# Performance work log

Measured on AMD Instinct MI355X. Metric: run time of the kernel, lower is better.

Reference implementation:

```python
import jax, jax.numpy as jnp
import numpy as np

N_NODES = 50000
HIDDEN = 128
N_REL = 9
N_LAYERS = 3
N_EDGES = 600000


def setup_inputs() -> dict:
    key = jax.random.key(0)
    k1, k2, k3, k4, k5 = jax.random.split(key, 5)
    edge_index = jax.random.randint(k1, (2, N_EDGES), 0, N_NODES, dtype=jnp.int64 if jax.config.jax_enable_x64 else jnp.int32)
    edge_type = jax.random.randint(k2, (N_EDGES,), 0, N_REL, dtype=edge_index.dtype)
    embeddings = jax.random.uniform(k3, (N_NODES, HIDDEN), dtype=jnp.float32)
    weights = jax.random.uniform(k4, (N_LAYERS, N_REL, HIDDEN, HIDDEN), dtype=jnp.float32)
    biases = jax.random.uniform(k5, (N_LAYERS, N_REL, HIDDEN), dtype=jnp.float32)
    return {"edge_index": edge_index, "edge_type": edge_type,
            "embeddings": embeddings, "weights": weights, "biases": biases}


def reference(edge_index, edge_type, embeddings, weights, biases):
    # RGCN: per relation r, messages = emb[src] @ W[l,r] + b[l,r], scatter-summed
    # into dest. Equivalent vectorized form: precompute X = emb @ W for all
    # relations ([R,N,E]), then a single gather + segment_sum over edges.
    L = weights.shape[0]
    N = embeddings.shape[0]
    dest = edge_index[0]
    src = edge_index[1]
    out = embeddings
    for l in range(L):
        X = jnp.einsum('ne,ref->rnf', out, weights[l])        # [R, N, E]
        msg = X[edge_type, src] + biases[l][edge_type]        # [num_edges, E]
        hidden = jax.ops.segment_sum(msg, dest, num_segments=N)  # [N, E]
        if l + 1 < L:
            hidden = jax.nn.relu(hidden)
        out = hidden
    return out
```

## Files before the change

### kernel.cpp

```cpp
#include <hip/hip_runtime.h>

#define NNODES 50000
#define HID 128
#define NREL 9
#define NLAYERS 3
#define NEDGES 600000

#define NBINS (NREL * NNODES)
#define SCAN_CHUNK 1024
#define NBLK ((NBINS + SCAN_CHUNK - 1) / SCAN_CHUNK)

#define KTOT (NREL * HID)
#define GM2 32
#define FPITCH 136

typedef __attribute__((ext_vector_type(8))) short short8;
typedef __attribute__((ext_vector_type(4))) float f32x4;

__device__ __forceinline__ short f2bf(float f) {
    union { float f; unsigned u; } c; c.f = f;
    unsigned r = c.u + 0x7fff + ((c.u >> 16) & 1);
    return (short)(r >> 16);
}
__device__ __forceinline__ float bf2f(short v) {
    return __uint_as_float(((unsigned)(unsigned short)v) << 16);
}


__global__ void hist2_kernel(const int* __restrict__ dst, const int* __restrict__ etype,
                             int* __restrict__ bins) {
    int e = blockIdx.x * blockDim.x + threadIdx.x;
    if (e < NEDGES) {
        int bin = etype[e] * NNODES + dst[e];
        atomicAdd(&bins[bin], 1);
    }
}

__global__ __launch_bounds__(256) void scan_pass1(const int* __restrict__ bins,
                                                  int* __restrict__ blocksum) {
    __shared__ int red[256];
    int b = blockIdx.x, t = threadIdx.x;
    int i0 = b * SCAN_CHUNK + t * 4;
    int s = 0;
#pragma unroll
    for (int k = 0; k < 4; k++)
        if (i0 + k < NBINS) s += bins[i0 + k];
    red[t] = s;
    __syncthreads();
    for (int off = 128; off > 0; off >>= 1) {
        if (t < off) red[t] += red[t + off];
        __syncthreads();
    }
    if (t == 0) blocksum[b] = red[0];
}

__global__ __launch_bounds__(512) void scan_pass2(const int* __restrict__ blocksum,
                                                  int* __restrict__ blockoff,
                                                  int* __restrict__ rowptr) {
    __shared__ int s[512];
    int t = threadIdx.x;
    int v = (t < NBLK) ? blocksum[t] : 0;
    s[t] = v;
    __syncthreads();
    for (int off = 1; off < 512; off <<= 1) {
        int x = (t >= off) ? s[t - off] : 0;
        __syncthreads();
        s[t] += x;
        __syncthreads();
    }
    if (t < NBLK) blockoff[t] = s[t] - v;
    if (t == 0) rowptr[NBINS] = NEDGES;
}

__global__ __launch_bounds__(256) void scan_pass3(const int* __restrict__ bins,
                                                  const int* __restrict__ blockoff,
                                                  int* __restrict__ rowptr,
                                                  int* __restrict__ cursor) {
    __shared__ int sc[256];
    int b = blockIdx.x, t = threadIdx.x;
    int i0 = b * SCAN_CHUNK + t * 4;
    int v[4], p[4];
    int s = 0;
#pragma unroll
    for (int k = 0; k < 4; k++) {
        v[k] = (i0 + k < NBINS) ? bins[i0 + k] : 0;
        p[k] = s;
        s += v[k];
    }
    sc[t] = s;
    __syncthreads();
    for (int off = 1; off < 256; off <<= 1) {
        int x = (t >= off) ? sc[t - off] : 0;
        __syncthreads();
        sc[t] += x;
        __syncthreads();
    }
    int base = blockoff[b] + (sc[t] - s);
#pragma unroll
    for (int k = 0; k < 4; k++) {
        if (i0 + k < NBINS) {
            rowptr[i0 + k] = base + p[k];
            cursor[i0 + k] = base + p[k];
        }
    }
}

__global__ void place_kernel(const int* __restrict__ dst, const int* __restrict__ src,
                             const int* __restrict__ etype,
                             int* __restrict__ cursor, int* __restrict__ bsrc) {
    int e = blockIdx.x * blockDim.x + threadIdx.x;
    if (e < NEDGES) {
        int bin = etype[e] * NNODES + dst[e];
        int pos = atomicAdd(&cursor[bin], 1);
        bsrc[pos] = src[e];
    }
}


__global__ __launch_bounds__(256) void convert_w(const float* __restrict__ W,
                                                 short* __restrict__ Wt2) {
    int lr = blockIdx.x;
    int l = lr / NREL, r = lr - l * NREL;
    const float* w = W + (size_t)lr * HID * HID;
    short* o = Wt2 + (size_t)l * HID * KTOT;
    int tid = threadIdx.x;
#pragma unroll 4
    for (int i = 0; i < 64; i++) {
        int elem = i * 256 + tid;
        int kk = elem >> 7, n = elem & 127;
        o[(size_t)n * KTOT + r * HID + kk] = f2bf(w[elem]);
    }
}

__global__ __launch_bounds__(256) void convert_emb(const float* __restrict__ E,
                                                   short* __restrict__ Ebf) {
    int gid = blockIdx.x * blockDim.x + threadIdx.x;
    const float* p = E + (size_t)gid * 8;
    float4 v0 = *(const float4*)p;
    float4 v1 = *(const float4*)(p + 4);
    short8 o = {f2bf(v0.x), f2bf(v0.y), f2bf(v0.z), f2bf(v0.w),
                f2bf(v1.x), f2bf(v1.y), f2bf(v1.z), f2bf(v1.w)};
    *(short8*)(Ebf + (size_t)gid * 8) = o;
}


__global__ __launch_bounds__(256, 4) void fused_kernel(const short* __restrict__ Hin,
                                                       const short* __restrict__ Wt2l,
                                                       const float* __restrict__ Bias,
                                                       const int* __restrict__ rowptr,
                                                       const int* __restrict__ bsrc,
                                                       short* __restrict__ HoutBf,
                                                       float* __restrict__ HoutF,
                                                       int last) {
    __shared__ short As[2][GM2 * FPITCH];
    __shared__ int   rp_s[NREL * (GM2 + 1)];
    __shared__ float bias_s[NREL * HID];

    int tid  = threadIdx.x;
    int wave = tid >> 6, lane = tid & 63;
    int lm = lane & 15, lq = lane >> 4;
    int row0 = blockIdx.x * GM2;
    int n0   = wave * 32;

    for (int i = tid; i < NREL * (GM2 + 1); i += 256) {
        int r = i / (GM2 + 1), o = i - r * (GM2 + 1);
        int d = row0 + o; if (d > NNODES) d = NNODES;
        rp_s[i] = rowptr[r * NNODES + d];
    }
    for (int i = tid; i < NREL * HID; i += 256) bias_s[i] = Bias[i];

    int grow = tid >> 3;
    int gcc  = tid & 3;
    gcc = tid & 7;

    f32x4 acc[2][2];
#pragma unroll
    for (int a = 0; a < 2; a++)
#pragma unroll
        for (int b = 0; b < 2; b++) acc[a][b] = (f32x4){0.f, 0.f, 0.f, 0.f};

    __syncthreads();

    const short* wb = Wt2l + (size_t)(n0 + lm) * KTOT + lq * 8;

    for (int r = 0; r < NREL; r++) {
        short* Ap = &As[r & 1][0];

        short8 bfr[2][4];
#pragma unroll
        for (int nt = 0; nt < 2; nt++)
#pragma unroll
            for (int ks = 0; ks < 4; ks++)
                bfr[nt][ks] = *(const short8*)(wb + (size_t)nt * 16 * KTOT + r * HID + ks * 32);

        int rs = rp_s[r * (GM2 + 1) + grow];
        int re = rp_s[r * (GM2 + 1) + grow + 1];
        float ga[16];
#pragma unroll
        for (int i = 0; i < 16; i++) ga[i] = 0.f;
        int j = rs;
        while (j + 1 < re) {
            int s0 = bsrc[j];
            int s1 = bsrc[j + 1];
            const short8* h0 = (const short8*)(Hin + (size_t)s0 * HID + gcc * 16);
            const short8* h1 = (const short8*)(Hin + (size_t)s1 * HID + gcc * 16);
            short8 a0 = h0[0], a1 = h0[1];
            short8 b0 = h1[0], b1 = h1[1];
#pragma unroll
            for (int i = 0; i < 8; i++) {
                ga[i]     += bf2f(a0[i]) + bf2f(b0[i]);
                ga[i + 8] += bf2f(a1[i]) + bf2f(b1[i]);
            }
            j += 2;
        }
        if (j < re) {
            int s0 = bsrc[j];
            const short8* h0 = (const short8*)(Hin + (size_t)s0 * HID + gcc * 16);
            short8 a0 = h0[0], a1 = h0[1];
#pragma unroll
            for (int i = 0; i < 8; i++) {
                ga[i]     += bf2f(a0[i]);
                ga[i + 8] += bf2f(a1[i]);
            }
        }

        {
            short8 o0, o1;
#pragma unroll
            for (int i = 0; i < 8; i++) {
                o0[i] = f2bf(ga[i]);
                o1[i] = f2bf(ga[i + 8]);
            }
            short8* ap = (short8*)&Ap[grow * FPITCH + gcc * 16];
            ap[0] = o0; ap[1] = o1;
        }
        __syncthreads();

#pragma unroll
        for (int ks = 0; ks < 4; ks++) {
            short8 af0 = *(const short8*)&Ap[(lm     ) * FPITCH + ks * 32 + lq * 8];
            short8 af1 = *(const short8*)&Ap[(lm + 16) * FPITCH + ks * 32 + lq * 8];
            __builtin_amdgcn_s_setprio(1);
            acc[0][0] = __builtin_amdgcn_mfma_f32_16x16x32_bf16(af0, bfr[0][ks], acc[0][0], 0, 0, 0);
            acc[1][0] = __builtin_amdgcn_mfma_f32_16x16x32_bf16(af1, bfr[0][ks], acc[1][0], 0, 0, 0);
            acc[0][1] = __builtin_amdgcn_mfma_f32_16x16x32_bf16(af0, bfr[1][ks], acc[0][1], 0, 0, 0);
            acc[1][1] = __builtin_amdgcn_mfma_f32_16x16x32_bf16(af1, bfr[1][ks], acc[1][1], 0, 0, 0);
            __builtin_amdgcn_s_setprio(0);
        }
    }

    __syncthreads();

    if (!last) {
        short (*Et)[FPITCH] = (short(*)[FPITCH])&As[0][0];
#pragma unroll
        for (int mt = 0; mt < 2; mt++) {
#pragma unroll
            for (int reg = 0; reg < 4; reg++) {
                int rl = mt * 16 + lq * 4 + reg;
                float cr[NREL];
#pragma unroll
                for (int rr = 0; rr < NREL; rr++)
                    cr[rr] = (float)(rp_s[rr * (GM2 + 1) + rl + 1] - rp_s[rr * (GM2 + 1) + rl]);
#pragma unroll
                for (int nt = 0; nt < 2; nt++) {
                    int n = n0 + nt * 16 + lm;
                    float b = 0.f;
#pragma unroll
                    for (int rr = 0; rr < NREL; rr++) b += cr[rr] * bias_s[rr * HID + n];
                    float o = fmaxf(acc[mt][nt][reg] + b, 0.f);
                    Et[rl][n] = f2bf(o);
                }
            }
        }
        __syncthreads();
#pragma unroll
        for (int i = 0; i < 2; i++) {
            int p = i * 256 + tid;
            int row = p >> 4, cc = p & 15;
            int d = row0 + row;
            if (d < NNODES)
                *(short8*)(HoutBf + (size_t)d * HID + cc * 8) = *(const short8*)&Et[row][cc * 8];
        }
    } else {
#pragma unroll
        for (int mt = 0; mt < 2; mt++) {
#pragma unroll
            for (int reg = 0; reg < 4; reg++) {
                int rl = mt * 16 + lq * 4 + reg;
                int d  = row0 + rl;
                if (d >= NNODES) continue;
                float cr[NREL];
#pragma unroll
                for (int rr = 0; rr < NREL; rr++)
                    cr[rr] = (float)(rp_s[rr * (GM2 + 1) + rl + 1] - rp_s[rr * (GM2 + 1) + rl]);
#pragma unroll
                for (int nt = 0; nt < 2; nt++) {
                    int n = n0 + nt * 16 + lm;
                    float b = 0.f;
#pragma unroll
                    for (int rr = 0; rr < NREL; rr++) b += cr[rr] * bias_s[rr * HID + n];
                    HoutF[(size_t)d * HID + n] = acc[mt][nt][reg] + b;
                }
            }
        }
    }
}


extern "C" void kernel_launch(void* const* d_in, const int* in_sizes, int n_in,
                              void* d_out, int out_size, void* d_ws, size_t ws_size,
                              hipStream_t stream) {
    const int*   edge_index = (const int*)d_in[0];
    const int*   etype      = (const int*)d_in[1];
    const float* emb        = (const float*)d_in[2];
    const float* W          = (const float*)d_in[3];
    const float* Bias       = (const float*)d_in[4];
    float*       out        = (float*)d_out;

    const int* dst  = edge_index;
    const int* srcA = edge_index + NEDGES;

    short* Ebf  = (short*)d_ws;
    short* HbfA = Ebf  + (size_t)NNODES * HID;
    short* HbfB = HbfA + (size_t)NNODES * HID;
    short* Wt2  = HbfB + (size_t)NNODES * HID;
    int*   bsrc     = (int*)(Wt2 + (size_t)NLAYERS * HID * KTOT);
    int*   bins     = bsrc + NEDGES;
    int*   cursor   = bins + NBINS;
    int*   rowptr   = cursor + NBINS;
    int*   blocksum = rowptr + NBINS + 1;
    int*   blockoff = blocksum + NBLK;

    hipMemsetAsync(bins, 0, NBINS * sizeof(int), stream);
    hist2_kernel<<<(NEDGES + 255) / 256, 256, 0, stream>>>(dst, etype, bins);
    scan_pass1<<<NBLK, 256, 0, stream>>>(bins, blocksum);
    scan_pass2<<<1, 512, 0, stream>>>(blocksum, blockoff, rowptr);
    scan_pass3<<<NBLK, 256, 0, stream>>>(bins, blockoff, rowptr, cursor);
    place_kernel<<<(NEDGES + 255) / 256, 256, 0, stream>>>(dst, srcA, etype, cursor, bsrc);
    convert_w<<<NLAYERS * NREL, 256, 0, stream>>>(W, Wt2);
    convert_emb<<<(NNODES * HID / 8) / 256, 256, 0, stream>>>(emb, Ebf);

    const int nblocks = (NNODES + GM2 - 1) / GM2;
    const short* Hin = Ebf;
    for (int l = 0; l < NLAYERS; l++) {
        int last = (l + 1 == NLAYERS);
        short* Hout = (l == 0) ? HbfA : HbfB;
        if (l == 2) Hout = HbfA;
        const short* Wtl = Wt2 + (size_t)l * HID * KTOT;
        const float* Bl  = Bias + (size_t)l * NREL * HID;
        fused_kernel<<<nblocks, 256, 0, stream>>>(
            Hin, Wtl, Bl, rowptr, bsrc, Hout, out, last);
        Hin = Hout;
    }
}
```

Measured before the change: 471.2 us.

## Gather edges per relation into LDS with float atomics instead of per-row loops

The fused layer kernel changes from giving each destination row one thread team that walks its own edge list to having 32 teams stride across all edges of the relation inside the block's row range. Each team adds its edge's features into an fp32 LDS tile with atomics, and the next edge is prefetched one step ahead. The goal is to remove load imbalance from uneven row degrees and to expose more memory-level parallelism in the gather. The cost is a bdst array written by place_kernel, LDS float atomics, a zeroing pass for every relation tile, and fp32-to-bf16 conversion at fragment load. Separately, the histogram, embedding-convert and weight-convert kernels are merged into one launch.

```diff
diff --git a/kernel.cpp b/kernel.cpp
--- a/kernel.cpp
+++ b/kernel.cpp
@@ -12,7 +12,13 @@
 
 #define KTOT (NREL * HID)
 #define GM2 32
+#define AP 132
+#define AWORDS (GM2 * AP)
 #define FPITCH 136
+
+#define HIST_BLKS ((NEDGES + 255) / 256)
+#define EMB_BLKS  ((NNODES * HID / 8) / 256)
+#define W_BLKS    (NLAYERS * NREL)
 
 typedef __attribute__((ext_vector_type(8))) short short8;
 typedef __attribute__((ext_vector_type(4))) float f32x4;
@@ -27,14 +33,42 @@
 }
 
 
-__global__ void hist2_kernel(const int* __restrict__ dst, const int* __restrict__ etype,
-                             int* __restrict__ bins) {
-    int e = blockIdx.x * blockDim.x + threadIdx.x;
-    if (e < NEDGES) {
-        int bin = etype[e] * NNODES + dst[e];
-        atomicAdd(&bins[bin], 1);
-    }
-}
+__global__ __launch_bounds__(256) void prep_kernel(const int* __restrict__ dst,
+                                                   const int* __restrict__ etype,
+                                                   int* __restrict__ bins,
+                                                   const float* __restrict__ E,
+                                                   short* __restrict__ Ebf,
+                                                   const float* __restrict__ W,
+                                                   short* __restrict__ Wt2) {
+    int b = blockIdx.x, tid = threadIdx.x;
+    if (b < HIST_BLKS) {
+        int e = b * 256 + tid;
+        if (e < NEDGES) {
+            int bin = etype[e] * NNODES + dst[e];
+            atomicAdd(&bins[bin], 1);
+        }
+    } else if (b < HIST_BLKS + EMB_BLKS) {
+        int gid = (b - HIST_BLKS) * 256 + tid;
+        const float* p = E + (size_t)gid * 8;
+        float4 v0 = *(const float4*)p;
+        float4 v1 = *(const float4*)(p + 4);
+        short8 o = {f2bf(v0.x), f2bf(v0.y), f2bf(v0.z), f2bf(v0.w),
+                    f2bf(v1.x), f2bf(v1.y), f2bf(v1.z), f2bf(v1.w)};
+        *(short8*)(Ebf + (size_t)gid * 8) = o;
+    } else {
+        int lr = b - HIST_BLKS - EMB_BLKS;
+        int l = lr / NREL, r = lr - l * NREL;
+        const float* w = W + (size_t)lr * HID * HID;
+        short* o = Wt2 + (size_t)l * HID * KTOT;
+#pragma unroll 4
+        for (int i = 0; i < 64; i++) {
+            int elem = i * 256 + tid;
+            int kk = elem >> 7, n = elem & 127;
+            o[(size_t)n * KTOT + r * HID + kk] = f2bf(w[elem]);
+        }
+    }
+}
+
 
 __global__ __launch_bounds__(256) void scan_pass1(const int* __restrict__ bins,
                                                   int* __restrict__ blocksum) {
@@ -107,40 +141,16 @@
 
 __global__ void place_kernel(const int* __restrict__ dst, const int* __restrict__ src,
                              const int* __restrict__ etype,
-                             int* __restrict__ cursor, int* __restrict__ bsrc) {
+                             int* __restrict__ cursor,
+                             int* __restrict__ bsrc, int* __restrict__ bdst) {
     int e = blockIdx.x * blockDim.x + threadIdx.x;
     if (e < NEDGES) {
-        int bin = etype[e] * NNODES + dst[e];
+        int d = dst[e];
+        int bin = etype[e] * NNODES + d;
         int pos = atomicAdd(&cursor[bin], 1);
         bsrc[pos] = src[e];
-    }
-}
-
-
-__global__ __launch_bounds__(256) void convert_w(const float* __restrict__ W,
-                                                 short* __restrict__ Wt2) {
-    int lr = blockIdx.x;
-    int l = lr / NREL, r = lr - l * NREL;
-    const float* w = W + (size_t)lr * HID * HID;
-    short* o = Wt2 + (size_t)l * HID * KTOT;
-    int tid = threadIdx.x;
-#pragma unroll 4
-    for (int i = 0; i < 64; i++) {
-        int elem = i * 256 + tid;
-        int kk = elem >> 7, n = elem & 127;
-        o[(size_t)n * KTOT + r * HID + kk] = f2bf(w[elem]);
-    }
-}
-
-__global__ __launch_bounds__(256) void convert_emb(const float* __restrict__ E,
-                                                   short* __restrict__ Ebf) {
-    int gid = blockIdx.x * blockDim.x + threadIdx.x;
-    const float* p = E + (size_t)gid * 8;
-    float4 v0 = *(const float4*)p;
-    float4 v1 = *(const float4*)(p + 4);
-    short8 o = {f2bf(v0.x), f2bf(v0.y), f2bf(v0.z), f2bf(v0.w),
-                f2bf(v1.x), f2bf(v1.y), f2bf(v1.z), f2bf(v1.w)};
-    *(short8*)(Ebf + (size_t)gid * 8) = o;
+        bdst[pos] = d;
+    }
 }
 
 
@@ -149,10 +159,11 @@
                                                        const float* __restrict__ Bias,
                                                        const int* __restrict__ rowptr,
                                                        const int* __restrict__ bsrc,
+                                                       const int* __restrict__ bdst,
                                                        short* __restrict__ HoutBf,
                                                        float* __restrict__ HoutF,
                                                        int last) {
-    __shared__ short As[2][GM2 * FPITCH];
+    __shared__ float AsF[2][AWORDS];
     __shared__ int   rp_s[NREL * (GM2 + 1)];
     __shared__ float bias_s[NREL * HID];
 
@@ -161,6 +172,22 @@
     int lm = lane & 15, lq = lane >> 4;
     int row0 = blockIdx.x * GM2;
     int n0   = wave * 32;
+    int team = tid >> 3;
+    int cg   = tid & 7;
+
+    int rsb0 = rowptr[row0];
+    int rebB = rowptr[(row0 + GM2 > NNODES) ? NNODES : (row0 + GM2)];
+    int e_st = rsb0 + team;
+    int stv  = (e_st < rebB);
+    int st_row = 0;
+    short8 sv0, sv1;
+    if (stv) {
+        int s = bsrc[e_st];
+        st_row = bdst[e_st] - row0;
+        const short* hb = Hin + (size_t)s * HID + cg * 8;
+        sv0 = *(const short8*)hb;
+        sv1 = *(const short8*)(hb + 64);
+    }
 
     for (int i = tid; i < NREL * (GM2 + 1); i += 256) {
         int r = i / (GM2 + 1), o = i - r * (GM2 + 1);
@@ -168,10 +195,11 @@
         rp_s[i] = rowptr[r * NNODES + d];
     }
     for (int i = tid; i < NREL * HID; i += 256) bias_s[i] = Bias[i];
-
-    int grow = tid >> 3;
-    int gcc  = tid & 3;
-    gcc = tid & 7;
+    {
+        float4 z = {0.f, 0.f, 0.f, 0.f};
+        float4* zp = (float4*)&AsF[0][0];
+        for (int i = tid; i < 2 * AWORDS / 4; i += 256) zp[i] = z;
+    }
 
     f32x4 acc[2][2];
 #pragma unroll
@@ -179,12 +207,12 @@
 #pragma unroll
         for (int b = 0; b < 2; b++) acc[a][b] = (f32x4){0.f, 0.f, 0.f, 0.f};
 
+    const short* wb = Wt2l + (size_t)(n0 + lm) * KTOT + lq * 8;
+
     __syncthreads();
 
-    const short* wb = Wt2l + (size_t)(n0 + lm) * KTOT + lq * 8;
-
     for (int r = 0; r < NREL; r++) {
-        short* Ap = &As[r & 1][0];
+        float* Ap = &AsF[r & 1][0];
 
         short8 bfr[2][4];
 #pragma unroll
@@ -193,53 +221,53 @@
             for (int ks = 0; ks < 4; ks++)
                 bfr[nt][ks] = *(const short8*)(wb + (size_t)nt * 16 * KTOT + r * HID + ks * 32);
 
-        int rs = rp_s[r * (GM2 + 1) + grow];
-        int re = rp_s[r * (GM2 + 1) + grow + 1];
-        float ga[16];
-#pragma unroll
-        for (int i = 0; i < 16; i++) ga[i] = 0.f;
-        int j = rs;
-        while (j + 1 < re) {
-            int s0 = bsrc[j];
-            int s1 = bsrc[j + 1];
-            const short8* h0 = (const short8*)(Hin + (size_t)s0 * HID + gcc * 16);
-            const short8* h1 = (const short8*)(Hin + (size_t)s1 * HID + gcc * 16);
-            short8 a0 = h0[0], a1 = h0[1];
-            short8 b0 = h1[0], b1 = h1[1];
-#pragma unroll
-            for (int i = 0; i < 8; i++) {
-                ga[i]     += bf2f(a0[i]) + bf2f(b0[i]);
-                ga[i + 8] += bf2f(a1[i]) + bf2f(b1[i]);
+        int reb = rp_s[r * (GM2 + 1) + GM2];
+        int e = e_st;
+        while (stv) {
+            int e2 = e + 32;
+            int nv = (e2 < reb);
+            int row2 = 0; short8 w0, w1;
+            if (nv) {
+                int s2 = bsrc[e2];
+                row2 = bdst[e2] - row0;
+                const short* hb = Hin + (size_t)s2 * HID + cg * 8;
+                w0 = *(const short8*)hb;
+                w1 = *(const short8*)(hb + 64);
             }
-            j += 2;
-        }
-        if (j < re) {
-            int s0 = bsrc[j];
-            const short8* h0 = (const short8*)(Hin + (size_t)s0 * HID + gcc * 16);
-            short8 a0 = h0[0], a1 = h0[1];
-#pragma unroll
-            for (int i = 0; i < 8; i++) {
-                ga[i]     += bf2f(a0[i]);
-                ga[i + 8] += bf2f(a1[i]);
+            float* base = Ap + st_row * AP + cg * 8;
+#pragma unroll
+            for (int i = 0; i < 8; i++) atomicAdd(&base[i], bf2f(sv0[i]));
+#pragma unroll
+            for (int i = 0; i < 8; i++) atomicAdd(&base[64 + i], bf2f(sv1[i]));
+            stv = nv;
+            if (nv) { st_row = row2; sv0 = w0; sv1 = w1; e = e2; }
+        }
+        __syncthreads();
+
+        if (r + 1 < NREL) {
+            int nrsb = rp_s[(r + 1) * (GM2 + 1)];
+            int nreb = rp_s[(r + 1) * (GM2 + 1) + GM2];
+            e_st = nrsb + team;
+            stv  = (e_st < nreb);
+            if (stv) {
+                int s = bsrc[e_st];
+                st_row = bdst[e_st] - row0;
+                const short* hb = Hin + (size_t)s * HID + cg * 8;
+                sv0 = *(const short8*)hb;
+                sv1 = *(const short8*)(hb + 64);
             }
         }
 
-        {
-            short8 o0, o1;
-#pragma unroll
-            for (int i = 0; i < 8; i++) {
-                o0[i] = f2bf(ga[i]);
-                o1[i] = f2bf(ga[i + 8]);
-            }
-            short8* ap = (short8*)&Ap[grow * FPITCH + gcc * 16];
-            ap[0] = o0; ap[1] = o1;
-        }
-        __syncthreads();
-
 #pragma unroll
         for (int ks = 0; ks < 4; ks++) {
-            short8 af0 = *(const short8*)&Ap[(lm     ) * FPITCH + ks * 32 + lq * 8];
-            short8 af1 = *(const short8*)&Ap[(lm + 16) * FPITCH + ks * 32 + lq * 8];
+            const float4* pa0 = (const float4*)&Ap[lm * AP + ks * 32 + lq * 8];
+            float4 x0 = pa0[0], x1 = pa0[1];
+            const float4* pa1 = (const float4*)&Ap[(lm + 16) * AP + ks * 32 + lq * 8];
+            float4 y0 = pa1[0], y1 = pa1[1];
+            short8 af0 = {f2bf(x0.x), f2bf(x0.y), f2bf(x0.z), f2bf(x0.w),
+                          f2bf(x1.x), f2bf(x1.y), f2bf(x1.z), f2bf(x1.w)};
+            short8 af1 = {f2bf(y0.x), f2bf(y0.y), f2bf(y0.z), f2bf(y0.w),
+                          f2bf(y1.x), f2bf(y1.y), f2bf(y1.z), f2bf(y1.w)};
             __builtin_amdgcn_s_setprio(1);
             acc[0][0] = __builtin_amdgcn_mfma_f32_16x16x32_bf16(af0, bfr[0][ks], acc[0][0], 0, 0, 0);
             acc[1][0] = __builtin_amdgcn_mfma_f32_16x16x32_bf16(af1, bfr[0][ks], acc[1][0], 0, 0, 0);
@@ -247,12 +275,17 @@
             acc[1][1] = __builtin_amdgcn_mfma_f32_16x16x32_bf16(af1, bfr[1][ks], acc[1][1], 0, 0, 0);
             __builtin_amdgcn_s_setprio(0);
         }
-    }
-
-    __syncthreads();
+        __syncthreads();
+
+        if (r + 2 < NREL) {
+            float4 z = {0.f, 0.f, 0.f, 0.f};
+            float4* zp = (float4*)Ap;
+            for (int i = tid; i < AWORDS / 4; i += 256) zp[i] = z;
+        }
+    }
 
     if (!last) {
-        short (*Et)[FPITCH] = (short(*)[FPITCH])&As[0][0];
+        short (*Et)[FPITCH] = (short(*)[FPITCH])&AsF[0][0];
 #pragma unroll
         for (int mt = 0; mt < 2; mt++) {
 #pragma unroll
@@ -326,20 +359,20 @@
     short* HbfB = HbfA + (size_t)NNODES * HID;
     short* Wt2  = HbfB + (size_t)NNODES * HID;
     int*   bsrc     = (int*)(Wt2 + (size_t)NLAYERS * HID * KTOT);
-    int*   bins     = bsrc + NEDGES;
+    int*   bdst     = bsrc + NEDGES;
+    int*   bins     = bdst + NEDGES;
     int*   cursor   = bins + NBINS;
     int*   rowptr   = cursor + NBINS;
     int*   blocksum = rowptr + NBINS + 1;
     int*   blockoff = blocksum + NBLK;
 
     hipMemsetAsync(bins, 0, NBINS * sizeof(int), stream);
-    hist2_kernel<<<(NEDGES + 255) / 256, 256, 0, stream>>>(dst, etype, bins);
+    prep_kernel<<<HIST_BLKS + EMB_BLKS + W_BLKS, 256, 0, stream>>>(
+        dst, etype, bins, emb, Ebf, W, Wt2);
     scan_pass1<<<NBLK, 256, 0, stream>>>(bins, blocksum);
     scan_pass2<<<1, 512, 0, stream>>>(blocksum, blockoff, rowptr);
     scan_pass3<<<NBLK, 256, 0, stream>>>(bins, blockoff, rowptr, cursor);
-    place_kernel<<<(NEDGES + 255) / 256, 256, 0, stream>>>(dst, srcA, etype, cursor, bsrc);
-    convert_w<<<NLAYERS * NREL, 256, 0, stream>>>(W, Wt2);
-    convert_emb<<<(NNODES * HID / 8) / 256, 256, 0, stream>>>(emb, Ebf);
+    place_kernel<<<(NEDGES + 255) / 256, 256, 0, stream>>>(dst, srcA, etype, cursor, bsrc, bdst);
 
     const int nblocks = (NNODES + GM2 - 1) / GM2;
     const short* Hin = Ebf;
@@ -350,7 +383,7 @@
         const short* Wtl = Wt2 + (size_t)l * HID * KTOT;
         const float* Bl  = Bias + (size_t)l * NREL * HID;
         fused_kernel<<<nblocks, 256, 0, stream>>>(
-            Hin, Wtl, Bl, rowptr, bsrc, Hout, out, last);
+            Hin, Wtl, Bl, rowptr, bsrc, bdst, Hout, out, last);
         Hin = Hout;
     }
 }
```

Result: slower. 1.612 ms (+242.2%).

## Gather all relations into LDS before one long MFMA loop; merge prep kernels

Applied to the files above, without the earlier changes.

The fused layer kernel now gathers and sums the neighbour rows for all nine relations into one large shared-memory tile first, using teams of four threads that each cover 32 columns and unroll four edges at a time. It then runs a single MFMA loop over the whole K=1152 dimension, where before it alternated gather, sync and MFMA per relation. This removes eight barriers per block and gives more memory-level parallelism in the gather, at the cost of about 74KB of LDS, which drops occupancy to two blocks per CU. The histogram, embedding conversion and weight conversion kernels are also merged into one launch to save launch overhead.

```diff
diff --git a/kernel.cpp b/kernel.cpp
--- a/kernel.cpp
+++ b/kernel.cpp
@@ -12,7 +12,12 @@
 
 #define KTOT (NREL * HID)
 #define GM2 32
+#define KPITCH 1160
 #define FPITCH 136
+
+#define HIST_BLKS ((NEDGES + 255) / 256)
+#define EMB_BLKS  ((NNODES * HID / 8) / 256)
+#define W_BLKS    (NLAYERS * NREL)
 
 typedef __attribute__((ext_vector_type(8))) short short8;
 typedef __attribute__((ext_vector_type(4))) float f32x4;
@@ -27,14 +32,42 @@
 }
 
 
-__global__ void hist2_kernel(const int* __restrict__ dst, const int* __restrict__ etype,
-                             int* __restrict__ bins) {
-    int e = blockIdx.x * blockDim.x + threadIdx.x;
-    if (e < NEDGES) {
-        int bin = etype[e] * NNODES + dst[e];
-        atomicAdd(&bins[bin], 1);
-    }
-}
+__global__ __launch_bounds__(256) void prep_kernel(const int* __restrict__ dst,
+                                                   const int* __restrict__ etype,
+                                                   int* __restrict__ bins,
+                                                   const float* __restrict__ E,
+                                                   short* __restrict__ Ebf,
+                                                   const float* __restrict__ W,
+                                                   short* __restrict__ Wt2) {
+    int b = blockIdx.x, tid = threadIdx.x;
+    if (b < HIST_BLKS) {
+        int e = b * 256 + tid;
+        if (e < NEDGES) {
+            int bin = etype[e] * NNODES + dst[e];
+            atomicAdd(&bins[bin], 1);
+        }
+    } else if (b < HIST_BLKS + EMB_BLKS) {
+        int gid = (b - HIST_BLKS) * 256 + tid;
+        const float* p = E + (size_t)gid * 8;
+        float4 v0 = *(const float4*)p;
+        float4 v1 = *(const float4*)(p + 4);
+        short8 o = {f2bf(v0.x), f2bf(v0.y), f2bf(v0.z), f2bf(v0.w),
+                    f2bf(v1.x), f2bf(v1.y), f2bf(v1.z), f2bf(v1.w)};
+        *(short8*)(Ebf + (size_t)gid * 8) = o;
+    } else {
+        int lr = b - HIST_BLKS - EMB_BLKS;
+        int l = lr / NREL, r = lr - l * NREL;
+        const float* w = W + (size_t)lr * HID * HID;
+        short* o = Wt2 + (size_t)l * HID * KTOT;
+#pragma unroll 4
+        for (int i = 0; i < 64; i++) {
+            int elem = i * 256 + tid;
+            int kk = elem >> 7, n = elem & 127;
+            o[(size_t)n * KTOT + r * HID + kk] = f2bf(w[elem]);
+        }
+    }
+}
+
 
 __global__ __launch_bounds__(256) void scan_pass1(const int* __restrict__ bins,
                                                   int* __restrict__ blocksum) {
@@ -117,34 +150,7 @@
 }
 
 
-__global__ __launch_bounds__(256) void convert_w(const float* __restrict__ W,
-                                                 short* __restrict__ Wt2) {
-    int lr = blockIdx.x;
-    int l = lr / NREL, r = lr - l * NREL;
-    const float* w = W + (size_t)lr * HID * HID;
-    short* o = Wt2 + (size_t)l * HID * KTOT;
-    int tid = threadIdx.x;
-#pragma unroll 4
-    for (int i = 0; i < 64; i++) {
-        int elem = i * 256 + tid;
-        int kk = elem >> 7, n = elem & 127;
-        o[(size_t)n * KTOT + r * HID + kk] = f2bf(w[elem]);
-    }
-}
-
-__global__ __launch_bounds__(256) void convert_emb(const float* __restrict__ E,
-                                                   short* __restrict__ Ebf) {
-    int gid = blockIdx.x * blockDim.x + threadIdx.x;
-    const float* p = E + (size_t)gid * 8;
-    float4 v0 = *(const float4*)p;
-    float4 v1 = *(const float4*)(p + 4);
-    short8 o = {f2bf(v0.x), f2bf(v0.y), f2bf(v0.z), f2bf(v0.w),
-                f2bf(v1.x), f2bf(v1.y), f2bf(v1.z), f2bf(v1.w)};
-    *(short8*)(Ebf + (size_t)gid * 8) = o;
-}
-
-
-__global__ __launch_bounds__(256, 4) void fused_kernel(const short* __restrict__ Hin,
+__global__ __launch_bounds__(256, 2) void fused_kernel(const short* __restrict__ Hin,
                                                        const short* __restrict__ Wt2l,
                                                        const float* __restrict__ Bias,
                                                        const int* __restrict__ rowptr,
@@ -152,7 +158,7 @@
                                                        short* __restrict__ HoutBf,
                                                        float* __restrict__ HoutF,
                                                        int last) {
-    __shared__ short As[2][GM2 * FPITCH];
+    __shared__ short As[GM2 * KPITCH];
     __shared__ int   rp_s[NREL * (GM2 + 1)];
     __shared__ float bias_s[NREL * HID];
 
@@ -168,10 +174,59 @@
         rp_s[i] = rowptr[r * NNODES + d];
     }
     for (int i = tid; i < NREL * HID; i += 256) bias_s[i] = Bias[i];
-
-    int grow = tid >> 3;
-    int gcc  = tid & 3;
-    gcc = tid & 7;
+    __syncthreads();
+
+    int team = tid >> 2;
+    int cg   = tid & 3;
+    int grow = team & 31;
+    int nbin = (team < 32) ? 5 : 4;
+    int r0g  = (team < 32) ? 0 : 1;
+    const short* hb = Hin + cg * 32;
+
+    for (int bj = 0; bj < nbin; bj++) {
+        int rr = r0g + bj * 2;
+        int rs = rp_s[rr * (GM2 + 1) + grow];
+        int re = rp_s[rr * (GM2 + 1) + grow + 1];
+        float a[32];
+#pragma unroll
+        for (int i = 0; i < 32; i++) a[i] = 0.f;
+
+        for (int i = rs; i < re; i += 4) {
+            int rem = re - i;
+            int i1 = (rem > 1) ? i + 1 : i;
+            int i2 = (rem > 2) ? i + 2 : i;
+            int i3 = (rem > 3) ? i + 3 : i;
+            int s0 = bsrc[i], s1 = bsrc[i1], s2 = bsrc[i2], s3 = bsrc[i3];
+            const short8* p0 = (const short8*)(hb + (size_t)s0 * HID);
+            const short8* p1 = (const short8*)(hb + (size_t)s1 * HID);
+            const short8* p2 = (const short8*)(hb + (size_t)s2 * HID);
+            const short8* p3 = (const short8*)(hb + (size_t)s3 * HID);
+            short8 v0[4] = {p0[0], p0[1], p0[2], p0[3]};
+            short8 v1[4] = {p1[0], p1[1], p1[2], p1[3]};
+            short8 v2[4] = {p2[0], p2[1], p2[2], p2[3]};
+            short8 v3[4] = {p3[0], p3[1], p3[2], p3[3]};
+            float m1 = (rem > 1) ? 1.f : 0.f;
+            float m2 = (rem > 2) ? 1.f : 0.f;
+            float m3 = (rem > 3) ? 1.f : 0.f;
+#pragma unroll
+            for (int q = 0; q < 4; q++)
+#pragma unroll
+                for (int k = 0; k < 8; k++) {
+                    float t0 = bf2f(v0[q][k]) + m1 * bf2f(v1[q][k]);
+                    float t1 = m2 * bf2f(v2[q][k]) + m3 * bf2f(v3[q][k]);
+                    a[q * 8 + k] += t0 + t1;
+                }
+        }
+        short8* ap = (short8*)&As[grow * KPITCH + rr * HID + cg * 32];
+#pragma unroll
+        for (int q = 0; q < 4; q++) {
+            short8 o;
+#pragma unroll
+            for (int k = 0; k < 8; k++) o[k] = f2bf(a[q * 8 + k]);
+            ap[q] = o;
+        }
+    }
+    __syncthreads();
 
     f32x4 acc[2][2];
 #pragma unroll
@@ -179,80 +234,26 @@
 #pragma unroll
         for (int b = 0; b < 2; b++) acc[a][b] = (f32x4){0.f, 0.f, 0.f, 0.f};
 
-    __syncthreads();
-
-    const short* wb = Wt2l + (size_t)(n0 + lm) * KTOT + lq * 8;
-
-    for (int r = 0; r < NREL; r++) {
-        short* Ap = &As[r & 1][0];
-
-        short8 bfr[2][4];
-#pragma unroll
-        for (int nt = 0; nt < 2; nt++)
-#pragma unroll
-            for (int ks = 0; ks < 4; ks++)
-                bfr[nt][ks] = *(const short8*)(wb + (size_t)nt * 16 * KTOT + r * HID + ks * 32);
-
-        int rs = rp_s[r * (GM2 + 1) + grow];
-        int re = rp_s[r * (GM2 + 1) + grow + 1];
-        float ga[16];
-#pragma unroll
-        for (int i = 0; i < 16; i++) ga[i] = 0.f;
-        int j = rs;
-        while (j + 1 < re) {
-            int s0 = bsrc[j];
-            int s1 = bsrc[j + 1];
-            const short8* h0 = (const short8*)(Hin + (size_t)s0 * HID + gcc * 16);
-            const short8* h1 = (const short8*)(Hin + (size_t)s1 * HID + gcc * 16);
-            short8 a0 = h0[0], a1 = h0[1];
-            short8 b0 = h1[0], b1 = h1[1];
-#pragma unroll
-            for (int i = 0; i < 8; i++) {
-                ga[i]     += bf2f(a0[i]) + bf2f(b0[i]);
-                ga[i + 8] += bf2f(a1[i]) + bf2f(b1[i]);
-            }
-            j += 2;
-        }
-        if (j < re) {
-            int s0 = bsrc[j];
-            const short8* h0 = (const short8*)(Hin + (size_t)s0 * HID + gcc * 16);
-            short8 a0 = h0[0], a1 = h0[1];
-#pragma unroll
-            for (int i = 0; i < 8; i++) {
-                ga[i]     += bf2f(a0[i]);
-                ga[i + 8] += bf2f(a1[i]);
-            }
-        }
-
-        {
-            short8 o0, o1;
-#pragma unroll
-            for (int i = 0; i < 8; i++) {
-                o0[i] = f2bf(ga[i]);
-                o1[i] = f2bf(ga[i + 8]);
-            }
-            short8* ap = (short8*)&Ap[grow * FPITCH + gcc * 16];
-            ap[0] = o0; ap[1] = o1;
-        }
-        __syncthreads();
-
-#pragma unroll
-        for (int ks = 0; ks < 4; ks++) {
-            short8 af0 = *(const short8*)&Ap[(lm     ) * FPITCH + ks * 32 + lq * 8];
-            short8 af1 = *(const short8*)&Ap[(lm + 16) * FPITCH + ks * 32 + lq * 8];
-            __builtin_amdgcn_s_setprio(1);
-            acc[0][0] = __builtin_amdgcn_mfma_f32_16x16x32_bf16(af0, bfr[0][ks], acc[0][0], 0, 0, 0);
-            acc[1][0] = __builtin_amdgcn_mfma_f32_16x16x32_bf16(af1, bfr[0][ks], acc[1][0], 0, 0, 0);
-            acc[0][1] = __builtin_amdgcn_mfma_f32_16x16x32_bf16(af0, bfr[1][ks], acc[0][1], 0, 0, 0);
-            acc[1][1] = __builtin_amdgcn_mfma_f32_16x16x32_bf16(af1, bfr[1][ks], acc[1][1], 0, 0, 0);
-            __builtin_amdgcn_s_setprio(0);
-        }
-    }
-
+    const short* wb0 = Wt2l + (size_t)(n0 + lm) * KTOT + lq * 8;
+    const short* wb1 = wb0 + (size_t)16 * KTOT;
+
+#pragma unroll 4
+    for (int kc = 0; kc < KTOT / 32; kc++) {
+        short8 b0 = *(const short8*)(wb0 + kc * 32);
+        short8 b1 = *(const short8*)(wb1 + kc * 32);
+        short8 a0 = *(const short8*)&As[(lm     ) * KPITCH + kc * 32 + lq * 8];
+        short8 a1 = *(const short8*)&As[(lm + 16) * KPITCH + kc * 32 + lq * 8];
+        __builtin_amdgcn_s_setprio(1);
+        acc[0][0] = __builtin_amdgcn_mfma_f32_16x16x32_bf16(a0, b0, acc[0][0], 0, 0, 0);
+        acc[1][0] = __builtin_amdgcn_mfma_f32_16x16x32_bf16(a1, b0, acc[1][0], 0, 0, 0);
+        acc[0][1] = __builtin_amdgcn_mfma_f32_16x16x32_bf16(a0, b1, acc[0][1], 0, 0, 0);
+        acc[1][1] = __builtin_amdgcn_mfma_f32_16x16x32_bf16(a1, b1, acc[1][1], 0, 0, 0);
+        __builtin_amdgcn_s_setprio(0);
+    }
     __syncthreads();
 
     if (!last) {
-        short (*Et)[FPITCH] = (short(*)[FPITCH])&As[0][0];
+        short (*Et)[FPITCH] = (short(*)[FPITCH])&As[0];
 #pragma unroll
         for (int mt = 0; mt < 2; mt++) {
 #pragma unroll
@@ -326,20 +327,19 @@
     short* HbfB = HbfA + (size_t)NNODES * HID;
     short* Wt2  = HbfB + (size_t)NNODES * HID;
     int*   bsrc     = (int*)(Wt2 + (size_t)NLAYERS * HID * KTOT);
-    int*   bins     = bsrc + NEDGES;
+    int*   bins     = bsrc + NEDGES + 8;
     int*   cursor   = bins + NBINS;
     int*   rowptr   = cursor + NBINS;
     int*   blocksum = rowptr + NBINS + 1;
     int*   blockoff = blocksum + NBLK;
 
     hipMemsetAsync(bins, 0, NBINS * sizeof(int), stream);
-    hist2_kernel<<<(NEDGES + 255) / 256, 256, 0, stream>>>(dst, etype, bins);
+    prep_kernel<<<HIST_BLKS + EMB_BLKS + W_BLKS, 256, 0, stream>>>(
+        dst, etype, bins, emb, Ebf, W, Wt2);
     scan_pass1<<<NBLK, 256, 0, stream>>>(bins, blocksum);
     scan_pass2<<<1, 512, 0, stream>>>(blocksum, blockoff, rowptr);
     scan_pass3<<<NBLK, 256, 0, stream>>>(bins, blockoff, rowptr, cursor);
     place_kernel<<<(NEDGES + 255) / 256, 256, 0, stream>>>(dst, srcA, etype, cursor, bsrc);
-    convert_w<<<NLAYERS * NREL, 256, 0, stream>>>(W, Wt2);
-    convert_emb<<<(NNODES * HID / 8) / 256, 256, 0, stream>>>(emb, Ebf);
 
     const int nblocks = (NNODES + GM2 - 1) / GM2;
     const short* Hin = Ebf;
```

New measurement: 492.5 us. 1.05x slower.

## Merge prep kernels and prefetch edge indices with 4-way unrolled gather

Applied to the files above, without the earlier changes.

Folds the histogram, embedding conversion and weight conversion kernels into one launch to cut launch overhead. The fused layer kernel now prefetches the first four source indices of the next relation's segment before the barrier, and gathers four neighbour rows per iteration with masked accumulation instead of two. This is meant to expose more memory-level parallelism in the latency-bound gather. In exchange it adds redundant loads for short segments and padding reads past the end of bsrc.

```diff
diff --git a/kernel.cpp b/kernel.cpp
--- a/kernel.cpp
+++ b/kernel.cpp
@@ -14,6 +14,10 @@
 #define GM2 32
 #define FPITCH 136
 
+#define HIST_BLKS ((NEDGES + 255) / 256)
+#define EMB_BLKS  ((NNODES * HID / 8) / 256)
+#define W_BLKS    (NLAYERS * NREL)
+
 typedef __attribute__((ext_vector_type(8))) short short8;
 typedef __attribute__((ext_vector_type(4))) float f32x4;
 
@@ -27,14 +31,42 @@
 }
 
 
-__global__ void hist2_kernel(const int* __restrict__ dst, const int* __restrict__ etype,
-                             int* __restrict__ bins) {
-    int e = blockIdx.x * blockDim.x + threadIdx.x;
-    if (e < NEDGES) {
-        int bin = etype[e] * NNODES + dst[e];
-        atomicAdd(&bins[bin], 1);
-    }
-}
+__global__ __launch_bounds__(256) void prep_kernel(const int* __restrict__ dst,
+                                                   const int* __restrict__ etype,
+                                                   int* __restrict__ bins,
+                                                   const float* __restrict__ E,
+                                                   short* __restrict__ Ebf,
+                                                   const float* __restrict__ W,
+                                                   short* __restrict__ Wt2) {
+    int b = blockIdx.x, tid = threadIdx.x;
+    if (b < HIST_BLKS) {
+        int e = b * 256 + tid;
+        if (e < NEDGES) {
+            int bin = etype[e] * NNODES + dst[e];
+            atomicAdd(&bins[bin], 1);
+        }
+    } else if (b < HIST_BLKS + EMB_BLKS) {
+        int gid = (b - HIST_BLKS) * 256 + tid;
+        const float* p = E + (size_t)gid * 8;
+        float4 v0 = *(const float4*)p;
+        float4 v1 = *(const float4*)(p + 4);
+        short8 o = {f2bf(v0.x), f2bf(v0.y), f2bf(v0.z), f2bf(v0.w),
+                    f2bf(v1.x), f2bf(v1.y), f2bf(v1.z), f2bf(v1.w)};
+        *(short8*)(Ebf + (size_t)gid * 8) = o;
+    } else {
+        int lr = b - HIST_BLKS - EMB_BLKS;
+        int l = lr / NREL, r = lr - l * NREL;
+        const float* w = W + (size_t)lr * HID * HID;
+        short* o = Wt2 + (size_t)l * HID * KTOT;
+#pragma unroll 4
+        for (int i = 0; i < 64; i++) {
+            int elem = i * 256 + tid;
+            int kk = elem >> 7, n = elem & 127;
+            o[(size_t)n * KTOT + r * HID + kk] = f2bf(w[elem]);
+        }
+    }
+}
+
 
 __global__ __launch_bounds__(256) void scan_pass1(const int* __restrict__ bins,
                                                   int* __restrict__ blocksum) {
@@ -114,33 +146,6 @@
         int pos = atomicAdd(&cursor[bin], 1);
         bsrc[pos] = src[e];
     }
-}
-
-
-__global__ __launch_bounds__(256) void convert_w(const float* __restrict__ W,
-                                                 short* __restrict__ Wt2) {
-    int lr = blockIdx.x;
-    int l = lr / NREL, r = lr - l * NREL;
-    const float* w = W + (size_t)lr * HID * HID;
-    short* o = Wt2 + (size_t)l * HID * KTOT;
-    int tid = threadIdx.x;
-#pragma unroll 4
-    for (int i = 0; i < 64; i++) {
-        int elem = i * 256 + tid;
-        int kk = elem >> 7, n = elem & 127;
-        o[(size_t)n * KTOT + r * HID + kk] = f2bf(w[elem]);
-    }
-}
-
-__global__ __launch_bounds__(256) void convert_emb(const float* __restrict__ E,
-                                                   short* __restrict__ Ebf) {
-    int gid = blockIdx.x * blockDim.x + threadIdx.x;
-    const float* p = E + (size_t)gid * 8;
-    float4 v0 = *(const float4*)p;
-    float4 v1 = *(const float4*)(p + 4);
-    short8 o = {f2bf(v0.x), f2bf(v0.y), f2bf(v0.z), f2bf(v0.w),
-                f2bf(v1.x), f2bf(v1.y), f2bf(v1.z), f2bf(v1.w)};
-    *(short8*)(Ebf + (size_t)gid * 8) = o;
 }
 
 
@@ -161,6 +166,21 @@
     int lm = lane & 15, lq = lane >> 4;
     int row0 = blockIdx.x * GM2;
     int n0   = wave * 32;
+    int grow = tid >> 3;
+    int gcc  = tid & 7;
+
+    int d0  = row0 + grow;
+    int dc  = (d0     > NNODES) ? NNODES : d0;
+    int dc1 = (d0 + 1 > NNODES) ? NNODES : (d0 + 1);
+    int rs0 = rowptr[dc];
+    int re0 = rowptr[dc1];
+    int pf0 = 0, pf1 = 0, pf2 = 0, pf3 = 0;
+    if (rs0 < re0) {
+        pf0 = bsrc[rs0];
+        pf1 = bsrc[rs0 + 1];
+        pf2 = bsrc[rs0 + 2];
+        pf3 = bsrc[rs0 + 3];
+    }
 
     for (int i = tid; i < NREL * (GM2 + 1); i += 256) {
         int r = i / (GM2 + 1), o = i - r * (GM2 + 1);
@@ -169,10 +189,6 @@
     }
     for (int i = tid; i < NREL * HID; i += 256) bias_s[i] = Bias[i];
 
-    int grow = tid >> 3;
-    int gcc  = tid & 3;
-    gcc = tid & 7;
-
     f32x4 acc[2][2];
 #pragma unroll
     for (int a = 0; a < 2; a++)
@@ -182,6 +198,7 @@
     __syncthreads();
 
     const short* wb = Wt2l + (size_t)(n0 + lm) * KTOT + lq * 8;
+    const short* hb = Hin + gcc * 16;
 
     for (int r = 0; r < NREL; r++) {
         short* Ap = &As[r & 1][0];
@@ -198,29 +215,56 @@
         float ga[16];
 #pragma unroll
         for (int i = 0; i < 16; i++) ga[i] = 0.f;
+
         int j = rs;
-        while (j + 1 < re) {
+        if (j < re) {
+            int rem = re - j;
+            int s0 = pf0;
+            int s1 = (rem > 1) ? pf1 : s0;
+            int s2 = (rem > 2) ? pf2 : s0;
+            int s3 = (rem > 3) ? pf3 : s0;
+            const short8* p0 = (const short8*)(hb + (size_t)s0 * HID);
+            const short8* p1 = (const short8*)(hb + (size_t)s1 * HID);
+            const short8* p2 = (const short8*)(hb + (size_t)s2 * HID);
+            const short8* p3 = (const short8*)(hb + (size_t)s3 * HID);
+            short8 a0 = p0[0], a1 = p0[1];
+            short8 b0 = p1[0], b1 = p1[1];
+            short8 c0 = p2[0], c1 = p2[1];
+            short8 d0v = p3[0], d1v = p3[1];
+            float m1 = (rem > 1) ? 1.f : 0.f;
+            float m2 = (rem > 2) ? 1.f : 0.f;
+            float m3 = (rem > 3) ? 1.f : 0.f;
+#pragma unroll
+            for (int k = 0; k < 8; k++) {
+                ga[k]     += (bf2f(a0[k]) + m1 * bf2f(b0[k])) + (m2 * bf2f(c0[k]) + m3 * bf2f(d0v[k]));
+                ga[k + 8] += (bf2f(a1[k]) + m1 * bf2f(b1[k])) + (m2 * bf2f(c1[k]) + m3 * bf2f(d1v[k]));
+            }
+            j += 4;
+        }
+        for (; j < re; j += 4) {
+            int rem = re - j;
             int s0 = bsrc[j];
-            int s1 = bsrc[j + 1];
-            const short8* h0 = (const short8*)(Hin + (size_t)s0 * HID + gcc * 16);
-            const short8* h1 = (const short8*)(Hin + (size_t)s1 * HID + gcc * 16);
-            short8 a0 = h0[0], a1 = h0[1];
-            short8 b0 = h1[0], b1 = h1[1];
-#pragma unroll
-            for (int i = 0; i < 8; i++) {
-                ga[i]     += bf2f(a0[i]) + bf2f(b0[i]);
-                ga[i + 8] += bf2f(a1[i]) + bf2f(b1[i]);
-            }
-            j += 2;
-        }
-        if (j < re) {
-            int s0 = bsrc[j];
-            const short8* h0 = (const short8*)(Hin + (size_t)s0 * HID + gcc * 16);
-            short8 a0 = h0[0], a1 = h0[1];
-#pragma unroll
-            for (int i = 0; i < 8; i++) {
-                ga[i]     += bf2f(a0[i]);
-                ga[i + 8] += bf2f(a1[i]);
+            int t1 = bsrc[j + 1];
+            int t2 = bsrc[j + 2];
+            int t3 = bsrc[j + 3];
+            int s1 = (rem > 1) ? t1 : s0;
+            int s2 = (rem > 2) ? t2 : s0;
+            int s3 = (rem > 3) ? t3 : s0;
+            const short8* p0 = (const short8*)(hb + (size_t)s0 * HID);
+            const short8* p1 = (const short8*)(hb + (size_t)s1 * HID);
+            const short8* p2 = (const short8*)(hb + (size_t)s2 * HID);
+            const short8* p3 = (const short8*)(hb + (size_t)s3 * HID);
+            short8 a0 = p0[0], a1 = p0[1];
+            short8 b0 = p1[0], b1 = p1[1];
+            short8 c0 = p2[0], c1 = p2[1];
+            short8 d0v = p3[0], d1v = p3[1];
+            float m1 = (rem > 1) ? 1.f : 0.f;
+            float m2 = (rem > 2) ? 1.f : 0.f;
+            float m3 = (rem > 3) ? 1.f : 0.f;
+#pragma unroll
+            for (int k = 0; k < 8; k++) {
+                ga[k]     += (bf2f(a0[k]) + m1 * bf2f(b0[k])) + (m2 * bf2f(c0[k]) + m3 * bf2f(d0v[k]));
+                ga[k + 8] += (bf2f(a1[k]) + m1 * bf2f(b1[k])) + (m2 * bf2f(c1[k]) + m3 * bf2f(d1v[k]));
             }
         }
 
@@ -233,6 +277,17 @@
             }
             short8* ap = (short8*)&Ap[grow * FPITCH + gcc * 16];
             ap[0] = o0; ap[1] = o1;
+        }
+
+        if (r + 1 < NREL) {
+            int nrs = rp_s[(r + 1) * (GM2 + 1) + grow];
+            int nre = rp_s[(r + 1) * (GM2 + 1) + grow + 1];
+            if (nrs < nre) {
+                pf0 = bsrc[nrs];
+                pf1 = bsrc[nrs + 1];
+                pf2 = bsrc[nrs + 2];
+                pf3 = bsrc[nrs + 3];
+            }
         }
         __syncthreads();
 
@@ -326,20 +381,19 @@
     short* HbfB = HbfA + (size_t)NNODES * HID;
     short* Wt2  = HbfB + (size_t)NNODES * HID;
     int*   bsrc     = (int*)(Wt2 + (size_t)NLAYERS * HID * KTOT);
-    int*   bins     = bsrc + NEDGES;
+    int*   bins     = bsrc + NEDGES + 8;
     int*   cursor   = bins + NBINS;
     int*   rowptr   = cursor + NBINS;
     int*   blocksum = rowptr + NBINS + 1;
     int*   blockoff = blocksum + NBLK;
 
     hipMemsetAsync(bins, 0, NBINS * sizeof(int), stream);
-    hist2_kernel<<<(NEDGES + 255) / 256, 256, 0, stream>>>(dst, etype, bins);
+    prep_kernel<<<HIST_BLKS + EMB_BLKS + W_BLKS, 256, 0, stream>>>(
+        dst, etype, bins, emb, Ebf, W, Wt2);
     scan_pass1<<<NBLK, 256, 0, stream>>>(bins, blocksum);
     scan_pass2<<<1, 512, 0, stream>>>(blocksum, blockoff, rowptr);
     scan_pass3<<<NBLK, 256, 0, stream>>>(bins, blockoff, rowptr, cursor);
     place_kernel<<<(NEDGES + 255) / 256, 256, 0, stream>>>(dst, srcA, etype, cursor, bsrc);
-    convert_w<<<NLAYERS * NREL, 256, 0, stream>>>(W, Wt2);
-    convert_emb<<<(NNODES * HID / 8) / 256, 256, 0, stream>>>(emb, Ebf);
 
     const int nblocks = (NNODES + GM2 - 1) / GM2;
     const short* Hin = Ebf;
```

New measurement: 438.7 us. 6.9% less time.
